# Kernel tuning notes

Measured on AMD Instinct MI355X. Metric: run time of the kernel, lower is better.

The kernel has to match this reference:

```python
import jax, jax.numpy as jnp
import numpy as np

DIM = 1024
NUM_HEADS = 16
HEAD_DIM = DIM // NUM_HEADS


def setup_inputs() -> dict:
    key = jax.random.key(0)
    ks = jax.random.split(key, 5)
    B, T = 2, 2048
    x = jax.random.normal(ks[0], (B, T, DIM), dtype=jnp.float32)
    s = 1.0 / np.sqrt(DIM)
    W_qkv = jax.random.normal(ks[1], (DIM, 3 * DIM), dtype=jnp.float32) * s
    b_qkv = jnp.zeros((3 * DIM,), dtype=jnp.float32)
    W_out = jax.random.normal(ks[2], (DIM, DIM), dtype=jnp.float32) * s
    b_out = jnp.zeros((DIM,), dtype=jnp.float32)
    return {"x": x, "W_qkv": W_qkv, "b_qkv": b_qkv, "W_out": W_out, "b_out": b_out}


def reference(x, W_qkv, b_qkv, W_out, b_out):
    B, T, D = x.shape
    H, Hd = NUM_HEADS, HEAD_DIM
    qkv = x @ W_qkv + b_qkv                       # [B,T,3D]
    qkv = qkv.reshape(B, T, 3, H, Hd)
    q = jnp.transpose(qkv[:, :, 0], (0, 2, 1, 3))  # [B,H,T,Hd]
    k = jnp.transpose(qkv[:, :, 1], (0, 2, 1, 3))
    v = jnp.transpose(qkv[:, :, 2], (0, 2, 1, 3))
    att = jnp.einsum('bhqd,bhkd->bhqk', q, k) / np.sqrt(Hd)  # [B,H,T,T]
    causal = jnp.tril(jnp.ones((T, T), dtype=bool))
    att = jnp.where(causal[None, None], att, -jnp.inf)
    att = jax.nn.softmax(att, axis=-1)
    out = jnp.einsum('bhqk,bhkd->bhqd', att, v)   # [B,H,T,Hd]
    out = jnp.transpose(out, (0, 2, 1, 3)).reshape(B, T, D)
    return out @ W_out + b_out
```

## Files before the change

### kernel.cpp

```cpp
#include <hip/hip_runtime.h>
#include <hip/hip_bf16.h>

typedef unsigned short u16;
typedef __attribute__((ext_vector_type(8))) short short8;
typedef __attribute__((ext_vector_type(4))) float f32x4;
typedef __attribute__((ext_vector_type(4))) unsigned short u16x4;

#define LOG2E 1.44269504088896340736f
#define QSCALE_F 0.18033688011112042f


__device__ __forceinline__ void gl_lds16(const void* g, void* l) {
  __builtin_amdgcn_global_load_lds(
      (__attribute__((address_space(1))) void*)g,
      (__attribute__((address_space(3))) void*)l, 16, 0, 0);
}

__device__ __forceinline__ float exp2_fast(float x) {
#if __has_builtin(__builtin_amdgcn_exp2f)
  return __builtin_amdgcn_exp2f(x);
#else
  return exp2f(x);
#endif
}

__device__ __forceinline__ u16 f2bf(float f) {
  union { float f; unsigned int i; } v;
  v.f = f;
  unsigned int r = v.i + 0x7fffu + ((v.i >> 16) & 1u);
  return (u16)(r >> 16);
}

__device__ __forceinline__ unsigned int pack_bf2(float lo, float hi) {
  union { __hip_bfloat162 h2; unsigned int u; } c;
  c.h2 = __float22bfloat162_rn(make_float2(lo, hi));
  return c.u;
}


__global__ __launch_bounds__(256) void prep_kernel(
    const float4* __restrict__ x, u16x4* __restrict__ xb,
    const float* __restrict__ Wqkv, u16* __restrict__ WqkvT,
    const float* __restrict__ Wout, u16* __restrict__ WoutT) {
  __shared__ u16 t[64][65];
  int bid = blockIdx.x, tid = threadIdx.x;
  if (bid < 4096) {
    int i = bid * 256 + tid;
    float4 v = x[i];
    u16x4 o;
    o.x = f2bf(v.x); o.y = f2bf(v.y); o.z = f2bf(v.z); o.w = f2bf(v.w);
    xb[i] = o;
    return;
  }
  const float* W;
  u16* WT;
  int K = 1024, N, bxx, byy;
  if (bid < 4864) {
    int tt = bid - 4096;
    W = Wqkv; WT = WqkvT; N = 3072; bxx = tt % 48; byy = tt / 48;
  } else {
    int tt = bid - 4864;
    W = Wout; WT = WoutT; N = 1024; bxx = tt % 16; byy = tt / 16;
  }
  int r0 = byy * 64, c0 = bxx * 64;
  int tx = tid & 63, ty = tid >> 6;
  for (int r = ty; r < 64; r += 4)
    t[r][tx] = f2bf(W[(size_t)(r0 + r) * N + c0 + tx]);
  __syncthreads();
  for (int r = ty; r < 64; r += 4)
    WT[(size_t)(c0 + r) * K + r0 + tx] = t[tx][r];
}


template <bool OUT_F32, int BM, int BN, bool QSC>
__global__ __launch_bounds__(512, 1) void gemm8_kernel(
    const u16* __restrict__ A, const u16* __restrict__ Bt,
    const float* __restrict__ bias, void* __restrict__ Cout,
    int M, int N, int K) {
  constexpr int MI = BM / 32;
  constexpr int NJ = BN / 64;
  constexpr int CH_A = BM / 8;
  constexpr int CH_B = BN / 8;
  constexpr int PER_W = (CH_A + CH_B) / 8;
  __shared__ u16 LDS[2][(BM + BN) * 64];
  int tid = threadIdx.x;
  int w = tid >> 6, lane = tid & 63, l15 = lane & 15, quad = lane >> 4;
  int bid = blockIdx.y * gridDim.x + blockIdx.x;
  int swz = ((bid & 7) << 5) | (bid >> 3);
  int bx = swz % gridDim.x, by = swz / gridDim.x;
  int m0 = by * BM, n0 = bx * BN;
  int wm = (w & 1) * (BM / 2), wn = (w >> 1) * (BN / 4);

  f32x4 acc[MI][NJ];
#pragma unroll
  for (int i = 0; i < MI; ++i)
#pragma unroll
    for (int j = 0; j < NJ; ++j) {
      f32x4 z = {0.f, 0.f, 0.f, 0.f};
      acc[i][j] = z;
    }

  int r8 = lane >> 3;
  int sw = ((lane & 7) ^ r8) * 8;

  const u16* srcp[PER_W];
  int dsto[PER_W];
#pragma unroll
  for (int i = 0; i < PER_W; ++i) {
    int c = w * PER_W + i;
    if (c < CH_A) {
      srcp[i] = A + (size_t)(m0 + c * 8 + r8) * K + sw;
    } else {
      srcp[i] = Bt + (size_t)(n0 + (c - CH_A) * 8 + r8) * K + sw;
    }
    dsto[i] = c * 512;
  }

  int nt = K >> 6;
#pragma unroll
  for (int i = 0; i < PER_W; ++i) gl_lds16(srcp[i], &LDS[0][dsto[i]]);

  for (int t = 0; t < nt; ++t) {
    asm volatile("s_waitcnt vmcnt(0)" ::: "memory");
    __builtin_amdgcn_s_barrier();
    asm volatile("" ::: "memory");
    int cur = t & 1;
    if (t + 1 < nt) {
      int koff = (t + 1) << 6;
#pragma unroll
      for (int i = 0; i < PER_W; ++i)
        gl_lds16(srcp[i] + koff, &LDS[cur ^ 1][dsto[i]]);
    }
    const u16* As = &LDS[cur][0];
    const u16* Bs = &LDS[cur][CH_A * 512];
#pragma unroll
    for (int kh = 0; kh < 2; ++kh) {
      short8 af[MI], bf[NJ];
#pragma unroll
      for (int i = 0; i < MI; ++i) {
        int R = wm + i * 16 + l15;
        af[i] = *(const short8*)(As + R * 64 +
                                 ((kh * 32 + quad * 8) ^ ((R & 7) * 8)));
      }
#pragma unroll
      for (int j = 0; j < NJ; ++j) {
        int R = wn + j * 16 + l15;
        bf[j] = *(const short8*)(Bs + R * 64 +
                                 ((kh * 32 + quad * 8) ^ ((R & 7) * 8)));
      }
#pragma unroll
      for (int i = 0; i < MI; ++i)
#pragma unroll
        for (int j = 0; j < NJ; ++j)
          acc[i][j] = __builtin_amdgcn_mfma_f32_16x16x32_bf16(af[i], bf[j],
                                                              acc[i][j], 0, 0, 0);
    }
  }

  float bv[NJ];
#pragma unroll
  for (int j = 0; j < NJ; ++j) bv[j] = bias[n0 + wn + j * 16 + l15];
#pragma unroll
  for (int i = 0; i < MI; ++i)
#pragma unroll
    for (int j = 0; j < NJ; ++j) {
      int col = n0 + wn + j * 16 + l15;
      bool doq = QSC && (col < 1024);
#pragma unroll
      for (int r = 0; r < 4; ++r) {
        int row = m0 + wm + i * 16 + quad * 4 + r;
        float val = acc[i][j][r] + bv[j];
        if (doq) val *= QSCALE_F;
        if (OUT_F32)
          ((float*)Cout)[(size_t)row * N + col] = val;
        else
          ((u16*)Cout)[(size_t)row * N + col] = f2bf(val);
      }
    }
}


__global__ __launch_bounds__(512, 2) void flash_kernel(
    const u16* __restrict__ qkv, u16* __restrict__ att) {
  __shared__ unsigned int SH[28672];

  int tid = threadIdx.x;
  int w = tid >> 6, half = w >> 2, wq = w & 3;
  int lane = tid & 63, l15 = lane & 15, quad = lane >> 4;
  int bx = blockIdx.x;
  int p = bx >> 5, bh = bx & 31, b = bh >> 4, h = bh & 15;
  const int qs[2] = {15 - p, p};
  const int kmax0 = 2 * qs[0] + 1, kmax1 = 2 * p + 1;
  const int jmax = 16 - p;

  const u16* base = qkv + (size_t)b * 2048 * 3072 + h * 64;
  const u16* kb = base + 1024;
  const u16* vb = base + 2048;

  int ht = tid & 255;
  const int krow = ht >> 3, h7 = ht & 7;
  const int swk = (h7 ^ (krow & 7)) * 8;

  short8 qf[2][2][2];
#pragma unroll
  for (int t = 0; t < 2; ++t) {
    const u16* qtb = base + (size_t)(qs[t] * 128 + wq * 32 + l15) * 3072;
    qf[t][0][0] = *(const short8*)(qtb + quad * 8);
    qf[t][0][1] = *(const short8*)(qtb + 32 + quad * 8);
    qf[t][1][0] = *(const short8*)(qtb + 16 * 3072 + quad * 8);
    qf[t][1][1] = *(const short8*)(qtb + 16 * 3072 + 32 + quad * 8);
  }

  {
    unsigned int* Ks0 = SH + half * 2048;
    gl_lds16(kb + (size_t)(half * 64 + krow) * 3072 + swk,
             (char*)Ks0 + wq * 1024);
    gl_lds16(kb + (size_t)(half * 64 + 32 + krow) * 3072 + swk,
             (char*)Ks0 + 4096 + wq * 1024);
  }
  uint4 vr0 = *(const uint4*)(vb + (size_t)(half * 64 + 2 * krow) * 3072 + h7 * 8);
  uint4 vr1 = *(const uint4*)(vb + (size_t)(half * 64 + 2 * krow + 1) * 3072 + h7 * 8);

  f32x4 o[2][2][4];
#pragma unroll
  for (int t = 0; t < 2; ++t)
#pragma unroll
    for (int qsub = 0; qsub < 2; ++qsub)
#pragma unroll
      for (int jd = 0; jd < 4; ++jd) {
        f32x4 z = {0.f, 0.f, 0.f, 0.f};
        o[t][qsub][jd] = z;
      }
  f32x4 l4[2][2];
#pragma unroll
  for (int t = 0; t < 2; ++t)
#pragma unroll
    for (int qsub = 0; qsub < 2; ++qsub) {
      f32x4 z = {0.f, 0.f, 0.f, 0.f};
      l4[t][qsub] = z;
    }
  const short8 ones = {(short)0x3F80, (short)0x3F80, (short)0x3F80,
                       (short)0x3F80, (short)0x3F80, (short)0x3F80,
                       (short)0x3F80, (short)0x3F80};

  const int psw = (l15 & 7) << 2;
  unsigned int* Pw = SH + 20480 + w * 1024;

  int b3 = 0;
  for (int j = 0; j < jmax; ++j) {
    int kt = 2 * j + half;
    unsigned int* KsH = SH + b3 * 4096 + half * 2048;
    unsigned int* VtH = SH + 12288 + (j & 1) * 4096 + half * 2048;

    {
      const u16* av = (const u16*)&vr0;
      const u16* bvp = (const u16*)&vr1;
#pragma unroll
      for (int jj = 0; jj < 8; ++jj) {
        int d = h7 * 8 + jj;
        VtH[32 * d + (krow ^ ((jj ^ h7) << 2))] =
            (unsigned int)av[jj] | ((unsigned int)bvp[jj] << 16);
      }
    }

    int nb3 = b3 + 1;
    if (nb3 == 3) nb3 = 0;
    if (j + 1 < jmax) {
      int kn = (kt + 2) * 64;
      unsigned int* Ksn = SH + nb3 * 4096 + half * 2048;
      gl_lds16(kb + (size_t)(kn + krow) * 3072 + swk, (char*)Ksn + wq * 1024);
      gl_lds16(kb + (size_t)(kn + 32 + krow) * 3072 + swk,
               (char*)Ksn + 4096 + wq * 1024);
      vr0 = *(const uint4*)(vb + (size_t)(kn + 2 * krow) * 3072 + h7 * 8);
      vr1 = *(const uint4*)(vb + (size_t)(kn + 2 * krow + 1) * 3072 + h7 * 8);
    }
    b3 = nb3;

    asm volatile("s_waitcnt lgkmcnt(0)" ::: "memory");
    __builtin_amdgcn_s_barrier();
    asm volatile("" ::: "memory");

#pragma unroll
    for (int t = 0; t < 2; ++t) {
      int km = t ? kmax1 : kmax0;
      if (kt > km) continue;
      bool last = (kt == km);
      if (last && wq < 2) continue;
      bool domask = last || ((kt == km - 1) && wq < 2);
      int qloc = ((last ? (wq - 2) : wq) << 5) + l15;

      f32x4 s0[4], s1[4];
#pragma unroll
      for (int jn = 0; jn < 4; ++jn) {
        f32x4 z = {-16.f, -16.f, -16.f, -16.f};
        s0[jn] = z;
        s1[jn] = z;
      }
      __builtin_amdgcn_s_setprio(1);
#pragma unroll
      for (int ss = 0; ss < 2; ++ss) {
        short8 a0 = qf[t][0][ss];
        short8 a1 = qf[t][1][ss];
#pragma unroll
        for (int jn = 0; jn < 4; ++jn) {
          int row = jn * 16 + l15;
          short8 bk = *(const short8*)&KsH[32 * row + ((16 * ss + 4 * quad) ^
                                                       ((row & 7) << 2))];
          s0[jn] = __builtin_amdgcn_mfma_f32_16x16x32_bf16(bk, a0, s0[jn], 0, 0, 0);
          s1[jn] = __builtin_amdgcn_mfma_f32_16x16x32_bf16(bk, a1, s1[jn], 0, 0, 0);
        }
      }
      __builtin_amdgcn_s_setprio(0);

#pragma unroll
      for (int qsub = 0; qsub < 2; ++qsub) {
        int qq = qloc + qsub * 16;
        float pvv[4][4];
        if (domask) {
#pragma unroll
          for (int jn = 0; jn < 4; ++jn) {
            f32x4 sv = qsub ? s1[jn] : s0[jn];
#pragma unroll
            for (int r = 0; r < 4; ++r) {
              float e = exp2_fast(sv[r]);
              if (jn * 16 + quad * 4 + r > qq) e = 0.f;
              pvv[jn][r] = e;
            }
          }
        } else {
#pragma unroll
          for (int jn = 0; jn < 4; ++jn) {
            f32x4 sv = qsub ? s1[jn] : s0[jn];
#pragma unroll
            for (int r = 0; r < 4; ++r)
              pvv[jn][r] = exp2_fast(sv[r]);
          }
        }
#pragma unroll
        for (int jn = 0; jn < 4; ++jn) {
          uint2 dd = make_uint2(pack_bf2(pvv[jn][0], pvv[jn][1]),
                                pack_bf2(pvv[jn][2], pvv[jn][3]));
          *(uint2*)&Pw[qsub * 512 + 32 * l15 +
                       (((jn << 3) + (quad << 1)) ^ psw)] = dd;
        }
      }

      __builtin_amdgcn_s_setprio(1);
#pragma unroll
      for (int ss = 0; ss < 2; ++ss) {
        short8 pf0 = *(const short8*)&Pw[32 * l15 +
                                         (((ss << 4) + (quad << 2)) ^ psw)];
        short8 pf1 = *(const short8*)&Pw[512 + 32 * l15 +
                                         (((ss << 4) + (quad << 2)) ^ psw)];
        l4[t][0] = __builtin_amdgcn_mfma_f32_16x16x32_bf16(ones, pf0,
                                                           l4[t][0], 0, 0, 0);
        l4[t][1] = __builtin_amdgcn_mfma_f32_16x16x32_bf16(ones, pf1,
                                                           l4[t][1], 0, 0, 0);
#pragma unroll
        for (int jd = 0; jd < 4; ++jd) {
          int vrow = jd * 16 + l15;
          int f = (vrow & 7) ^ ((vrow >> 3) & 7);
          short8 bvv = *(const short8*)&VtH[32 * vrow +
                                            (((ss << 4) + (quad << 2)) ^ (f << 2))];
          o[t][0][jd] =
              __builtin_amdgcn_mfma_f32_16x16x32_bf16(bvv, pf0, o[t][0][jd], 0, 0, 0);
          o[t][1][jd] =
              __builtin_amdgcn_mfma_f32_16x16x32_bf16(bvv, pf1, o[t][1][jd], 0, 0, 0);
        }
      }
      __builtin_amdgcn_s_setprio(0);
    }
  }

  float lf[2][2];
#pragma unroll
  for (int t = 0; t < 2; ++t)
#pragma unroll
    for (int qsub = 0; qsub < 2; ++qsub) lf[t][qsub] = l4[t][qsub][0];

  float* OM = (float*)SH;
  float* LM = (float*)(SH + 8704);
  __syncthreads();
#pragma unroll
  for (int t = 0; t < 2; ++t) {
    if (half == 0) {
#pragma unroll
      for (int qsub = 0; qsub < 2; ++qsub) {
        int q = wq * 32 + qsub * 16 + l15;
#pragma unroll
        for (int jd = 0; jd < 4; ++jd)
          *(float4*)&OM[q * 68 + jd * 16 + quad * 4] = *(float4*)&o[t][qsub][jd];
        if (quad == 0) LM[q] = lf[t][qsub];
      }
    }
    __syncthreads();
    if (half == 1) {
#pragma unroll
      for (int qsub = 0; qsub < 2; ++qsub) {
        int q = wq * 32 + qsub * 16 + l15;
        float lr = lf[t][qsub] + LM[q];
        float inv = 1.f / lr;
        size_t row = (size_t)b * 2048 + qs[t] * 128 + q;
        u16* orow = att + row * 1024 + h * 64 + quad * 4;
#pragma unroll
        for (int jd = 0; jd < 4; ++jd) {
          float4 pa = *(float4*)&OM[q * 68 + jd * 16 + quad * 4];
          uint2 dd = make_uint2(pack_bf2((o[t][qsub][jd][0] + pa.x) * inv,
                                         (o[t][qsub][jd][1] + pa.y) * inv),
                                pack_bf2((o[t][qsub][jd][2] + pa.z) * inv,
                                         (o[t][qsub][jd][3] + pa.w) * inv));
          *(uint2*)(orow + jd * 16) = dd;
        }
      }
    }
    __syncthreads();
  }
}


extern "C" void kernel_launch(void* const* d_in, const int* in_sizes, int n_in,
                              void* d_out, int out_size, void* d_ws,
                              size_t ws_size, hipStream_t stream) {
  const float* x = (const float*)d_in[0];
  const float* Wqkv = (const float*)d_in[1];
  const float* bqkv = (const float*)d_in[2];
  const float* Wout = (const float*)d_in[3];
  const float* bout = (const float*)d_in[4];
  float* out = (float*)d_out;

  char* ws = (char*)d_ws;
  u16* WqkvT = (u16*)(ws);
  u16* WoutT = (u16*)(ws + 6291456);
  u16* qkv = (u16*)(ws + 8388608);
  u16* attn = (u16*)(ws + 33554432);
  u16* xb = (u16*)(ws + 41943040);

  prep_kernel<<<5120, 256, 0, stream>>>((const float4*)x, (u16x4*)xb, Wqkv,
                                        WqkvT, Wout, WoutT);
  gemm8_kernel<false, 256, 192, true><<<dim3(16, 16), 512, 0, stream>>>(
      xb, WqkvT, bqkv, (void*)qkv, 4096, 3072, 1024);
  flash_kernel<<<256, 512, 0, stream>>>(qkv, attn);
  gemm8_kernel<true, 128, 128, false><<<dim3(8, 32), 512, 0, stream>>>(
      attn, WoutT, bout, (void*)out, 4096, 1024, 1024);
}
```

Measured before the change: 159.7 us.

## Split flash attention query strips across separate waves in 1024-thread blocks

The flash kernel now launches 1024 threads per block. Each group of waves owns one of the two paired query strips, where before every wave looped over both strips in turn. Only strip-0 waves stage K/V tiles into shared memory, while all waves share the K/V buffers. This halves per-thread accumulator state and exposes the two strips as independent waves for latency hiding. In exchange it uses one block per CU with more LDS, and the waves of the shorter strip sit idle at barriers once their causal range ends.

```diff
diff --git a/kernel.cpp b/kernel.cpp
--- a/kernel.cpp
+++ b/kernel.cpp
@@ -180,65 +180,65 @@
 }
 
 
-__global__ __launch_bounds__(512, 2) void flash_kernel(
+__global__ __launch_bounds__(1024, 1) void flash_kernel(
     const u16* __restrict__ qkv, u16* __restrict__ att) {
-  __shared__ unsigned int SH[28672];
+  __shared__ unsigned int SH[36864];
 
   int tid = threadIdx.x;
-  int w = tid >> 6, half = w >> 2, wq = w & 3;
+  int w = tid >> 6;
+  int half = w >> 3;
+  int strip = (w >> 2) & 1;
+  int wq = w & 3;
   int lane = tid & 63, l15 = lane & 15, quad = lane >> 4;
   int bx = blockIdx.x;
   int p = bx >> 5, bh = bx & 31, b = bh >> 4, h = bh & 15;
-  const int qs[2] = {15 - p, p};
-  const int kmax0 = 2 * qs[0] + 1, kmax1 = 2 * p + 1;
+  const int st = strip ? p : (15 - p);
+  const int km = 2 * st + 1;
   const int jmax = 16 - p;
 
   const u16* base = qkv + (size_t)b * 2048 * 3072 + h * 64;
   const u16* kb = base + 1024;
   const u16* vb = base + 2048;
 
+  const bool stager = (strip == 0);
   int ht = tid & 255;
   const int krow = ht >> 3, h7 = ht & 7;
   const int swk = (h7 ^ (krow & 7)) * 8;
 
-  short8 qf[2][2][2];
-#pragma unroll
-  for (int t = 0; t < 2; ++t) {
-    const u16* qtb = base + (size_t)(qs[t] * 128 + wq * 32 + l15) * 3072;
-    qf[t][0][0] = *(const short8*)(qtb + quad * 8);
-    qf[t][0][1] = *(const short8*)(qtb + 32 + quad * 8);
-    qf[t][1][0] = *(const short8*)(qtb + 16 * 3072 + quad * 8);
-    qf[t][1][1] = *(const short8*)(qtb + 16 * 3072 + 32 + quad * 8);
-  }
-
+  short8 qf[2][2];
   {
+    const u16* qtb = base + (size_t)(st * 128 + wq * 32 + l15) * 3072;
+    qf[0][0] = *(const short8*)(qtb + quad * 8);
+    qf[0][1] = *(const short8*)(qtb + 32 + quad * 8);
+    qf[1][0] = *(const short8*)(qtb + 16 * 3072 + quad * 8);
+    qf[1][1] = *(const short8*)(qtb + 16 * 3072 + 32 + quad * 8);
+  }
+
+  uint4 vr0, vr1;
+  if (stager) {
     unsigned int* Ks0 = SH + half * 2048;
     gl_lds16(kb + (size_t)(half * 64 + krow) * 3072 + swk,
              (char*)Ks0 + wq * 1024);
     gl_lds16(kb + (size_t)(half * 64 + 32 + krow) * 3072 + swk,
              (char*)Ks0 + 4096 + wq * 1024);
-  }
-  uint4 vr0 = *(const uint4*)(vb + (size_t)(half * 64 + 2 * krow) * 3072 + h7 * 8);
-  uint4 vr1 = *(const uint4*)(vb + (size_t)(half * 64 + 2 * krow + 1) * 3072 + h7 * 8);
-
-  f32x4 o[2][2][4];
-#pragma unroll
-  for (int t = 0; t < 2; ++t)
-#pragma unroll
-    for (int qsub = 0; qsub < 2; ++qsub)
-#pragma unroll
-      for (int jd = 0; jd < 4; ++jd) {
-        f32x4 z = {0.f, 0.f, 0.f, 0.f};
-        o[t][qsub][jd] = z;
-      }
-  f32x4 l4[2][2];
-#pragma unroll
-  for (int t = 0; t < 2; ++t)
-#pragma unroll
-    for (int qsub = 0; qsub < 2; ++qsub) {
+    vr0 = *(const uint4*)(vb + (size_t)(half * 64 + 2 * krow) * 3072 + h7 * 8);
+    vr1 = *(const uint4*)(vb + (size_t)(half * 64 + 2 * krow + 1) * 3072 + h7 * 8);
+  }
+
+  f32x4 o[2][4];
+#pragma unroll
+  for (int qsub = 0; qsub < 2; ++qsub)
+#pragma unroll
+    for (int jd = 0; jd < 4; ++jd) {
       f32x4 z = {0.f, 0.f, 0.f, 0.f};
-      l4[t][qsub] = z;
-    }
+      o[qsub][jd] = z;
+    }
+  f32x4 l4[2];
+#pragma unroll
+  for (int qsub = 0; qsub < 2; ++qsub) {
+    f32x4 z = {0.f, 0.f, 0.f, 0.f};
+    l4[qsub] = z;
+  }
   const short8 ones = {(short)0x3F80, (short)0x3F80, (short)0x3F80,
                        (short)0x3F80, (short)0x3F80, (short)0x3F80,
                        (short)0x3F80, (short)0x3F80};
@@ -251,8 +251,10 @@
     int kt = 2 * j + half;
     unsigned int* KsH = SH + b3 * 4096 + half * 2048;
     unsigned int* VtH = SH + 12288 + (j & 1) * 4096 + half * 2048;
-
-    {
+    int nb3 = b3 + 1;
+    if (nb3 == 3) nb3 = 0;
+
+    if (stager) {
       const u16* av = (const u16*)&vr0;
       const u16* bvp = (const u16*)&vr1;
 #pragma unroll
@@ -261,18 +263,16 @@
         VtH[32 * d + (krow ^ ((jj ^ h7) << 2))] =
             (unsigned int)av[jj] | ((unsigned int)bvp[jj] << 16);
       }
-    }
-
-    int nb3 = b3 + 1;
-    if (nb3 == 3) nb3 = 0;
-    if (j + 1 < jmax) {
-      int kn = (kt + 2) * 64;
-      unsigned int* Ksn = SH + nb3 * 4096 + half * 2048;
-      gl_lds16(kb + (size_t)(kn + krow) * 3072 + swk, (char*)Ksn + wq * 1024);
-      gl_lds16(kb + (size_t)(kn + 32 + krow) * 3072 + swk,
-               (char*)Ksn + 4096 + wq * 1024);
-      vr0 = *(const uint4*)(vb + (size_t)(kn + 2 * krow) * 3072 + h7 * 8);
-      vr1 = *(const uint4*)(vb + (size_t)(kn + 2 * krow + 1) * 3072 + h7 * 8);
+      if (j + 1 < jmax) {
+        int kn = (kt + 2) * 64;
+        unsigned int* Ksn = SH + nb3 * 4096 + half * 2048;
+        gl_lds16(kb + (size_t)(kn + krow) * 3072 + swk,
+                 (char*)Ksn + wq * 1024);
+        gl_lds16(kb + (size_t)(kn + 32 + krow) * 3072 + swk,
+                 (char*)Ksn + 4096 + wq * 1024);
+        vr0 = *(const uint4*)(vb + (size_t)(kn + 2 * krow) * 3072 + h7 * 8);
+        vr1 = *(const uint4*)(vb + (size_t)(kn + 2 * krow + 1) * 3072 + h7 * 8);
+      }
     }
     b3 = nb3;
 
@@ -280,140 +280,127 @@
     __builtin_amdgcn_s_barrier();
     asm volatile("" ::: "memory");
 
-#pragma unroll
-    for (int t = 0; t < 2; ++t) {
-      int km = t ? kmax1 : kmax0;
-      if (kt > km) continue;
-      bool last = (kt == km);
-      if (last && wq < 2) continue;
-      bool domask = last || ((kt == km - 1) && wq < 2);
-      int qloc = ((last ? (wq - 2) : wq) << 5) + l15;
-
-      f32x4 s0[4], s1[4];
+    if (kt > km) continue;
+    bool last = (kt == km);
+    if (last && wq < 2) continue;
+    bool domask = last || ((kt == km - 1) && wq < 2);
+    int qloc = ((last ? (wq - 2) : wq) << 5) + l15;
+
+    f32x4 s0[4], s1[4];
+#pragma unroll
+    for (int jn = 0; jn < 4; ++jn) {
+      f32x4 z = {-16.f, -16.f, -16.f, -16.f};
+      s0[jn] = z;
+      s1[jn] = z;
+    }
+    __builtin_amdgcn_s_setprio(1);
+#pragma unroll
+    for (int ss = 0; ss < 2; ++ss) {
+      short8 a0 = qf[0][ss];
+      short8 a1 = qf[1][ss];
 #pragma unroll
       for (int jn = 0; jn < 4; ++jn) {
-        f32x4 z = {-16.f, -16.f, -16.f, -16.f};
-        s0[jn] = z;
-        s1[jn] = z;
-      }
-      __builtin_amdgcn_s_setprio(1);
-#pragma unroll
-      for (int ss = 0; ss < 2; ++ss) {
-        short8 a0 = qf[t][0][ss];
-        short8 a1 = qf[t][1][ss];
+        int row = jn * 16 + l15;
+        short8 bk = *(const short8*)&KsH[32 * row + ((16 * ss + 4 * quad) ^
+                                                     ((row & 7) << 2))];
+        s0[jn] = __builtin_amdgcn_mfma_f32_16x16x32_bf16(bk, a0, s0[jn], 0, 0, 0);
+        s1[jn] = __builtin_amdgcn_mfma_f32_16x16x32_bf16(bk, a1, s1[jn], 0, 0, 0);
+      }
+    }
+    __builtin_amdgcn_s_setprio(0);
+
+#pragma unroll
+    for (int qsub = 0; qsub < 2; ++qsub) {
+      int qq = qloc + qsub * 16;
+      float pvv[4][4];
+      if (domask) {
 #pragma unroll
         for (int jn = 0; jn < 4; ++jn) {
-          int row = jn * 16 + l15;
-          short8 bk = *(const short8*)&KsH[32 * row + ((16 * ss + 4 * quad) ^
-                                                       ((row & 7) << 2))];
-          s0[jn] = __builtin_amdgcn_mfma_f32_16x16x32_bf16(bk, a0, s0[jn], 0, 0, 0);
-          s1[jn] = __builtin_amdgcn_mfma_f32_16x16x32_bf16(bk, a1, s1[jn], 0, 0, 0);
-        }
-      }
-      __builtin_amdgcn_s_setprio(0);
-
-#pragma unroll
-      for (int qsub = 0; qsub < 2; ++qsub) {
-        int qq = qloc + qsub * 16;
-        float pvv[4][4];
-        if (domask) {
-#pragma unroll
-          for (int jn = 0; jn < 4; ++jn) {
-            f32x4 sv = qsub ? s1[jn] : s0[jn];
-#pragma unroll
-            for (int r = 0; r < 4; ++r) {
-              float e = exp2_fast(sv[r]);
-              if (jn * 16 + quad * 4 + r > qq) e = 0.f;
-              pvv[jn][r] = e;
-            }
-          }
-        } else {
-#pragma unroll
-          for (int jn = 0; jn < 4; ++jn) {
-            f32x4 sv = qsub ? s1[jn] : s0[jn];
-#pragma unroll
-            for (int r = 0; r < 4; ++r)
-              pvv[jn][r] = exp2_fast(sv[r]);
+          f32x4 sv = qsub ? s1[jn] : s0[jn];
+#pragma unroll
+          for (int r = 0; r < 4; ++r) {
+            float e = exp2_fast(sv[r]);
+            if (jn * 16 + quad * 4 + r > qq) e = 0.f;
+            pvv[jn][r] = e;
           }
         }
+      } else {
 #pragma unroll
         for (int jn = 0; jn < 4; ++jn) {
-          uint2 dd = make_uint2(pack_bf2(pvv[jn][0], pvv[jn][1]),
-                                pack_bf2(pvv[jn][2], pvv[jn][3]));
-          *(uint2*)&Pw[qsub * 512 + 32 * l15 +
-                       (((jn << 3) + (quad << 1)) ^ psw)] = dd;
+          f32x4 sv = qsub ? s1[jn] : s0[jn];
+#pragma unroll
+          for (int r = 0; r < 4; ++r)
+            pvv[jn][r] = exp2_fast(sv[r]);
         }
       }
-
-      __builtin_amdgcn_s_setprio(1);
-#pragma unroll
-      for (int ss = 0; ss < 2; ++ss) {
-        short8 pf0 = *(const short8*)&Pw[32 * l15 +
-                                         (((ss << 4) + (quad << 2)) ^ psw)];
-        short8 pf1 = *(const short8*)&Pw[512 + 32 * l15 +
-                                         (((ss << 4) + (quad << 2)) ^ psw)];
-        l4[t][0] = __builtin_amdgcn_mfma_f32_16x16x32_bf16(ones, pf0,
-                                                           l4[t][0], 0, 0, 0);
-        l4[t][1] = __builtin_amdgcn_mfma_f32_16x16x32_bf16(ones, pf1,
-                                                           l4[t][1], 0, 0, 0);
-#pragma unroll
-        for (int jd = 0; jd < 4; ++jd) {
-          int vrow = jd * 16 + l15;
-          int f = (vrow & 7) ^ ((vrow >> 3) & 7);
-          short8 bvv = *(const short8*)&VtH[32 * vrow +
-                                            (((ss << 4) + (quad << 2)) ^ (f << 2))];
-          o[t][0][jd] =
-              __builtin_amdgcn_mfma_f32_16x16x32_bf16(bvv, pf0, o[t][0][jd], 0, 0, 0);
-          o[t][1][jd] =
-              __builtin_amdgcn_mfma_f32_16x16x32_bf16(bvv, pf1, o[t][1][jd], 0, 0, 0);
-        }
-      }
-      __builtin_amdgcn_s_setprio(0);
-    }
-  }
-
-  float lf[2][2];
-#pragma unroll
-  for (int t = 0; t < 2; ++t)
-#pragma unroll
-    for (int qsub = 0; qsub < 2; ++qsub) lf[t][qsub] = l4[t][qsub][0];
+#pragma unroll
+      for (int jn = 0; jn < 4; ++jn) {
+        uint2 dd = make_uint2(pack_bf2(pvv[jn][0], pvv[jn][1]),
+                              pack_bf2(pvv[jn][2], pvv[jn][3]));
+        *(uint2*)&Pw[qsub * 512 + 32 * l15 +
+                     (((jn << 3) + (quad << 1)) ^ psw)] = dd;
+      }
+    }
+
+    __builtin_amdgcn_s_setprio(1);
+#pragma unroll
+    for (int ss = 0; ss < 2; ++ss) {
+      short8 pf0 = *(const short8*)&Pw[32 * l15 +
+                                       (((ss << 4) + (quad << 2)) ^ psw)];
+      short8 pf1 = *(const short8*)&Pw[512 + 32 * l15 +
+                                       (((ss << 4) + (quad << 2)) ^ psw)];
+      l4[0] = __builtin_amdgcn_mfma_f32_16x16x32_bf16(ones, pf0, l4[0], 0, 0, 0);
+      l4[1] = __builtin_amdgcn_mfma_f32_16x16x32_bf16(ones, pf1, l4[1], 0, 0, 0);
+#pragma unroll
+      for (int jd = 0; jd < 4; ++jd) {
+        int vrow = jd * 16 + l15;
+        int f = (vrow & 7) ^ ((vrow >> 3) & 7);
+        short8 bvv = *(const short8*)&VtH[32 * vrow +
+                                          (((ss << 4) + (quad << 2)) ^ (f << 2))];
+        o[0][jd] =
+            __builtin_amdgcn_mfma_f32_16x16x32_bf16(bvv, pf0, o[0][jd], 0, 0, 0);
+        o[1][jd] =
+            __builtin_amdgcn_mfma_f32_16x16x32_bf16(bvv, pf1, o[1][jd], 0, 0, 0);
+      }
+    }
+    __builtin_amdgcn_s_setprio(0);
+  }
+
+  float lf[2] = {l4[0][0], l4[1][0]};
 
   float* OM = (float*)SH;
-  float* LM = (float*)(SH + 8704);
+  float* LM = (float*)(SH + 17408);
   __syncthreads();
-#pragma unroll
-  for (int t = 0; t < 2; ++t) {
-    if (half == 0) {
-#pragma unroll
-      for (int qsub = 0; qsub < 2; ++qsub) {
-        int q = wq * 32 + qsub * 16 + l15;
-#pragma unroll
-        for (int jd = 0; jd < 4; ++jd)
-          *(float4*)&OM[q * 68 + jd * 16 + quad * 4] = *(float4*)&o[t][qsub][jd];
-        if (quad == 0) LM[q] = lf[t][qsub];
-      }
-    }
-    __syncthreads();
-    if (half == 1) {
-#pragma unroll
-      for (int qsub = 0; qsub < 2; ++qsub) {
-        int q = wq * 32 + qsub * 16 + l15;
-        float lr = lf[t][qsub] + LM[q];
-        float inv = 1.f / lr;
-        size_t row = (size_t)b * 2048 + qs[t] * 128 + q;
-        u16* orow = att + row * 1024 + h * 64 + quad * 4;
-#pragma unroll
-        for (int jd = 0; jd < 4; ++jd) {
-          float4 pa = *(float4*)&OM[q * 68 + jd * 16 + quad * 4];
-          uint2 dd = make_uint2(pack_bf2((o[t][qsub][jd][0] + pa.x) * inv,
-                                         (o[t][qsub][jd][1] + pa.y) * inv),
-                                pack_bf2((o[t][qsub][jd][2] + pa.z) * inv,
-                                         (o[t][qsub][jd][3] + pa.w) * inv));
-          *(uint2*)(orow + jd * 16) = dd;
-        }
-      }
-    }
-    __syncthreads();
+  if (half == 0) {
+#pragma unroll
+    for (int qsub = 0; qsub < 2; ++qsub) {
+      int q = wq * 32 + qsub * 16 + l15;
+#pragma unroll
+      for (int jd = 0; jd < 4; ++jd)
+        *(float4*)&OM[(strip * 128 + q) * 68 + jd * 16 + quad * 4] =
+            *(float4*)&o[qsub][jd];
+      if (quad == 0) LM[strip * 128 + q] = lf[qsub];
+    }
+  }
+  __syncthreads();
+  if (half == 1) {
+#pragma unroll
+    for (int qsub = 0; qsub < 2; ++qsub) {
+      int q = wq * 32 + qsub * 16 + l15;
+      float lr = lf[qsub] + LM[strip * 128 + q];
+      float inv = 1.f / lr;
+      size_t row = (size_t)b * 2048 + st * 128 + q;
+      u16* orow = att + row * 1024 + h * 64 + quad * 4;
+#pragma unroll
+      for (int jd = 0; jd < 4; ++jd) {
+        float4 pa = *(float4*)&OM[(strip * 128 + q) * 68 + jd * 16 + quad * 4];
+        uint2 dd = make_uint2(pack_bf2((o[0 + qsub][jd][0] + pa.x) * inv,
+                                       (o[qsub][jd][1] + pa.y) * inv),
+                              pack_bf2((o[qsub][jd][2] + pa.z) * inv,
+                                       (o[qsub][jd][3] + pa.w) * inv));
+        *(uint2*)(orow + jd * 16) = dd;
+      }
+    }
   }
 }
 
@@ -439,7 +426,7 @@
                                         WqkvT, Wout, WoutT);
   gemm8_kernel<false, 256, 192, true><<<dim3(16, 16), 512, 0, stream>>>(
       xb, WqkvT, bqkv, (void*)qkv, 4096, 3072, 1024);
-  flash_kernel<<<256, 512, 0, stream>>>(qkv, attn);
+  flash_kernel<<<256, 1024, 0, stream>>>(qkv, attn);
   gemm8_kernel<true, 128, 128, false><<<dim3(8, 32), 512, 0, stream>>>(
       attn, WoutT, bout, (void*)out, 4096, 1024, 1024);
 }
```

New measurement: 203.2 us. 27.2% more time.
